# Optimization experiments

Measured on AMD Instinct MI355X. Metric: run time of the kernel, lower is better.

Reference implementation:

```python
import jax, jax.numpy as jnp
import numpy as np

B, N, OUT = 128, 4096, 64
PHI = (64, 128, 256)
RHO = (256, 128)
FMIN = jnp.finfo(jnp.float32).min


def _linear_params(key, fan_in, fan_out):
    # torch nn.Linear default init: U(-1/sqrt(fan_in), 1/sqrt(fan_in))
    kw, kb = jax.random.split(key)
    bound = 1.0 / np.sqrt(fan_in)
    w = jax.random.uniform(kw, (fan_in, fan_out), jnp.float32, -bound, bound)
    b = jax.random.uniform(kb, (fan_out,), jnp.float32, -bound, bound)
    return w, b


def setup_inputs() -> dict:
    key = jax.random.key(0)
    ks = jax.random.split(key, 8)
    points = jax.random.normal(ks[0], (B, N, 2), jnp.float32)
    lengths = jax.random.randint(ks[1], (B,), 1, N + 1, jnp.int32)
    w1, b1 = _linear_params(ks[2], 2, PHI[0])
    w2, b2 = _linear_params(ks[3], PHI[0], PHI[1])
    w3, b3 = _linear_params(ks[4], PHI[1], PHI[2])
    r1w, r1b = _linear_params(ks[5], PHI[2], RHO[0])
    r2w, r2b = _linear_params(ks[6], RHO[0], RHO[1])
    r3w, r3b = _linear_params(ks[7], RHO[1], OUT)
    return {"points": points, "lengths": lengths,
            "w1": w1, "b1": b1, "w2": w2, "b2": b2, "w3": w3, "b3": b3,
            "r1w": r1w, "r1b": r1b, "r2w": r2w, "r2b": r2b, "r3w": r3w, "r3b": r3b}


def reference(points, lengths, w1, b1, w2, b2, w3, b3, r1w, r1b, r2w, r2b, r3w, r3b):
    # mask[b, n] = n < lengths[b]   (pad_sequence equivalent)
    mask = jnp.arange(N)[None, :] < lengths[:, None]            # [B, N]
    # phi MLP: per-point 2 -> 64 -> 128 -> 256 with ReLU
    h = jax.nn.relu(jnp.einsum('bnd,df->bnf', points, w1) + b1)
    h = jax.nn.relu(jnp.einsum('bnd,df->bnf', h, w2) + b2)
    h = jax.nn.relu(jnp.einsum('bnd,df->bnf', h, w3) + b3)       # [B, N, 256]
    # masked max-pool over points (padding -> dtype min, matching masked_fill)
    h = jnp.where(mask[:, :, None], h, FMIN)
    agg = jnp.max(h, axis=1)                                     # [B, 256]
    # rho MLP: 256 -> 256 -> 128 -> OUT (ReLU on hidden layers only)
    z = jax.nn.relu(agg @ r1w + r1b)
    z = jax.nn.relu(z @ r2w + r2b)
    return z @ r3w + r3b                                         # [B, OUT]
```

## Files before the change

### kernel.cpp

```cpp
#include <hip/hip_runtime.h>
#include <hip/hip_fp16.h>

#define BB   128
#define NN   4096
#define OUTD 64
#define P1   64
#define P2   128
#define P3   256
#define R1   256
#define R2   128
#define CHUNK 64

typedef _Float16 half8 __attribute__((ext_vector_type(8)));
typedef _Float16 half4 __attribute__((ext_vector_type(4)));
typedef float    f32x4 __attribute__((ext_vector_type(4)));

#define AGG_OFF 0
#define W2F_OFF (BB * P3 * 4)
#define W3F_OFF (W2F_OFF + P2 * P1 * 2)

__global__ void prep_kernel(const float* __restrict__ w2, const float* __restrict__ w3,
                            unsigned char* ws) {
  int idx = blockIdx.x * 256 + threadIdx.x;
  if (idx < BB * P3) ((unsigned*)(ws + AGG_OFF))[idx] = 0u;
  _Float16* W2F = (_Float16*)(ws + W2F_OFF);
  _Float16* W3F = (_Float16*)(ws + W3F_OFF);
  if (idx < P1 * P2) {
    int f = idx >> 9, rem = idx & 511, l = rem >> 3, j = rem & 7;
    int mt = f >> 1, ks = f & 1;
    int ch = mt * 16 + (l & 15), k = ks * 32 + (l >> 4) * 8 + j;
    W2F[idx] = (_Float16)w2[k * P2 + ch];
  }
  int i2 = idx - P1 * P2;
  if (i2 >= 0 && i2 < P2 * P3) {
    int f = i2 >> 9, rem = i2 & 511, l = rem >> 3, j = rem & 7;
    int mt = f >> 2, ks = f & 3;
    int ch = mt * 16 + (l & 15), k = ks * 32 + (l >> 4) * 8 + j;
    W3F[i2] = (_Float16)w3[k * P3 + ch];
  }
}

__launch_bounds__(256, 3)
__global__ void phi_kernel(const float* __restrict__ pts, const int* __restrict__ lengths,
                           const float* __restrict__ w1, const float* __restrict__ b1,
                           const float* __restrict__ b2, const float* __restrict__ b3,
                           unsigned char* ws) {
  __shared__ __align__(16) _Float16 sH1[8][CHUNK][8];
  __shared__ __align__(16) _Float16 sH2[16][CHUNK][8];

  int b  = blockIdx.y;
  int c0 = blockIdx.x * CHUNK;
  int len = lengths[b];
  if (c0 >= len) return;
  int v = min(CHUNK, len - c0);

  int t = threadIdx.x;
  int w = t >> 6, l = t & 63;
  int ml = l & 15, q = l >> 4;

  const half8* W2F = (const half8*)(ws + W2F_OFF);
  const half8* W3F = (const half8*)(ws + W3F_OFF);

  half8 a2[2][2];
#pragma unroll
  for (int mt2 = 0; mt2 < 2; ++mt2)
#pragma unroll
    for (int ks = 0; ks < 2; ++ks)
      a2[mt2][ks] = W2F[((w * 2 + mt2) * 2 + ks) * 64 + l];
  half8 a3c[4];
#pragma unroll
  for (int ks = 0; ks < 4; ++ks)
    a3c[ks] = W3F[((w * 4 + 0) * 4 + ks) * 64 + l];

  {
    const float2* Pp = (const float2*)pts + (size_t)b * NN + c0;
    float2 xy = Pp[l];
    half8 h8[2];
#pragma unroll
    for (int j = 0; j < 16; ++j) {
      int jj = w * 16 + j;
      float h = fmaf(xy.y, w1[P1 + jj], fmaf(xy.x, w1[jj], b1[jj]));
      h8[j >> 3][j & 7] = (_Float16)fmaxf(h, 0.f);
    }
    *(half8*)&sH1[w * 2][l][0]     = h8[0];
    *(half8*)&sH1[w * 2 + 1][l][0] = h8[1];
  }
  __syncthreads();

  {
    f32x4 acc2[2][4] = {};
#pragma unroll
    for (int ks = 0; ks < 2; ++ks) {
      half8 bf[4];
#pragma unroll
      for (int nt = 0; nt < 4; ++nt)
        bf[nt] = *(const half8*)&sH1[ks * 4 + q][nt * 16 + ml][0];
#pragma unroll
      for (int mt2 = 0; mt2 < 2; ++mt2)
#pragma unroll
        for (int nt = 0; nt < 4; ++nt)
          acc2[mt2][nt] = __builtin_amdgcn_mfma_f32_16x16x32_f16(
              a2[mt2][ks], bf[nt], acc2[mt2][nt], 0, 0, 0);
    }
#pragma unroll
    for (int mt2 = 0; mt2 < 2; ++mt2) {
      float4 b2v = *(const float4*)&b2[(w * 2 + mt2) * 16 + q * 4];
#pragma unroll
      for (int nt = 0; nt < 4; ++nt) {
        half4 hp;
        hp[0] = (_Float16)fmaxf(acc2[mt2][nt][0] + b2v.x, 0.f);
        hp[1] = (_Float16)fmaxf(acc2[mt2][nt][1] + b2v.y, 0.f);
        hp[2] = (_Float16)fmaxf(acc2[mt2][nt][2] + b2v.z, 0.f);
        hp[3] = (_Float16)fmaxf(acc2[mt2][nt][3] + b2v.w, 0.f);
        *(half4*)&sH2[(w * 2 + mt2) * 2 + (q >> 1)][nt * 16 + ml][(q & 1) * 4] = hp;
      }
    }
  }
  __syncthreads();

  unsigned* aggU = (unsigned*)(ws + AGG_OFF) + b * P3;
  for (int s = 0; s < 4; ++s) {
    half8 a3n[4];
    if (s < 3) {
#pragma unroll
      for (int ks = 0; ks < 4; ++ks)
        a3n[ks] = W3F[((w * 4 + s + 1) * 4 + ks) * 64 + l];
    }
    float4 b3v = *(const float4*)&b3[(w * 4 + s) * 16 + q * 4];
    f32x4 acc3[4] = {};
#pragma unroll
    for (int ks = 0; ks < 4; ++ks)
#pragma unroll
      for (int nt = 0; nt < 4; ++nt) {
        half8 bf = *(const half8*)&sH2[ks * 4 + q][nt * 16 + ml][0];
        acc3[nt] = __builtin_amdgcn_mfma_f32_16x16x32_f16(
            a3c[ks], bf, acc3[nt], 0, 0, 0);
      }
    float rm[4] = {0.f, 0.f, 0.f, 0.f};
    float bb[4] = {b3v.x, b3v.y, b3v.z, b3v.w};
#pragma unroll
    for (int nt = 0; nt < 4; ++nt) {
      bool ok = (nt * 16 + ml) < v;
#pragma unroll
      for (int r = 0; r < 4; ++r) {
        float val = fmaxf(acc3[nt][r] + bb[r], 0.f);
        if (ok) rm[r] = fmaxf(rm[r], val);
      }
    }
#pragma unroll
    for (int r = 0; r < 4; ++r) {
      float m = rm[r];
      m = fmaxf(m, __shfl_xor(m, 1));
      m = fmaxf(m, __shfl_xor(m, 2));
      m = fmaxf(m, __shfl_xor(m, 4));
      m = fmaxf(m, __shfl_xor(m, 8));
      if (ml == 0)
        atomicMax(&aggU[(w * 4 + s) * 16 + q * 4 + r], __float_as_uint(m));
    }
#pragma unroll
    for (int ks = 0; ks < 4; ++ks) a3c[ks] = a3n[ks];
  }
}

__global__ void rho_kernel(const unsigned char* __restrict__ ws,
                           const float* __restrict__ r1w, const float* __restrict__ r1b,
                           const float* __restrict__ r2w, const float* __restrict__ r2b,
                           const float* __restrict__ r3w, const float* __restrict__ r3b,
                           float* __restrict__ out) {
  __shared__ float sa[R1], sz1[R1], sz2[R2];
  int b = blockIdx.x, t = threadIdx.x;
  const float* agg = (const float*)(ws + AGG_OFF) + b * P3;
  sa[t] = agg[t];
  __syncthreads();
  {
    float p0 = 0.f, p1 = 0.f, p2 = 0.f, p3 = 0.f;
#pragma unroll 8
    for (int k = 0; k < 64; ++k) {
      p0 = fmaf(sa[k],       r1w[k * R1 + t],         p0);
      p1 = fmaf(sa[k + 64],  r1w[(k + 64) * R1 + t],  p1);
      p2 = fmaf(sa[k + 128], r1w[(k + 128) * R1 + t], p2);
      p3 = fmaf(sa[k + 192], r1w[(k + 192) * R1 + t], p3);
    }
    sz1[t] = fmaxf(r1b[t] + ((p0 + p1) + (p2 + p3)), 0.f);
  }
  __syncthreads();
  if (t < R2) {
    float p0 = 0.f, p1 = 0.f, p2 = 0.f, p3 = 0.f;
#pragma unroll 8
    for (int k = 0; k < 64; ++k) {
      p0 = fmaf(sz1[k],       r2w[k * R2 + t],         p0);
      p1 = fmaf(sz1[k + 64],  r2w[(k + 64) * R2 + t],  p1);
      p2 = fmaf(sz1[k + 128], r2w[(k + 128) * R2 + t], p2);
      p3 = fmaf(sz1[k + 192], r2w[(k + 192) * R2 + t], p3);
    }
    sz2[t] = fmaxf(r2b[t] + ((p0 + p1) + (p2 + p3)), 0.f);
  }
  __syncthreads();
  if (t < OUTD) {
    float p0 = 0.f, p1 = 0.f;
#pragma unroll 8
    for (int k = 0; k < 64; ++k) {
      p0 = fmaf(sz2[k],      r3w[k * OUTD + t],        p0);
      p1 = fmaf(sz2[k + 64], r3w[(k + 64) * OUTD + t], p1);
    }
    out[b * OUTD + t] = r3b[t] + p0 + p1;
  }
}

extern "C" void kernel_launch(void* const* d_in, const int* in_sizes, int n_in,
                              void* d_out, int out_size, void* d_ws, size_t ws_size,
                              hipStream_t stream) {
  const float* pts     = (const float*)d_in[0];
  const int*   lengths = (const int*)d_in[1];
  const float* w1  = (const float*)d_in[2];
  const float* b1  = (const float*)d_in[3];
  const float* w2  = (const float*)d_in[4];
  const float* b2  = (const float*)d_in[5];
  const float* w3  = (const float*)d_in[6];
  const float* b3  = (const float*)d_in[7];
  const float* r1w = (const float*)d_in[8];
  const float* r1b = (const float*)d_in[9];
  const float* r2w = (const float*)d_in[10];
  const float* r2b = (const float*)d_in[11];
  const float* r3w = (const float*)d_in[12];
  const float* r3b = (const float*)d_in[13];
  unsigned char* ws = (unsigned char*)d_ws;

  prep_kernel<<<160, 256, 0, stream>>>(w2, w3, ws);
  phi_kernel<<<dim3(NN / CHUNK, BB), 256, 0, stream>>>(pts, lengths, w1, b1, b2, b3, ws);
  rho_kernel<<<BB, 256, 0, stream>>>(ws, r1w, r1b, r2w, r2b, r3w, r3b, (float*)d_out);
}
```

Measured before the change: 145.9 us.

## Fuse rho MLP into phi kernel via last-block-done counter per batch

Removes the separate rho kernel launch. Each phi block increments a per-batch atomic counter after its atomicMax updates, and the last block for that batch reads the aggregated vector and runs the three rho layers in reused shared memory. The layer-2 MFMA loop is also restructured to keep fewer accumulators live, and launch bounds are raised to 4 waves per SIMD for occupancy. The trade-offs are an added threadfence and atomic on every block, and a serialized rho tail running inside one block per batch.

```diff
diff --git a/kernel.cpp b/kernel.cpp
--- a/kernel.cpp
+++ b/kernel.cpp
@@ -18,11 +18,13 @@
 #define AGG_OFF 0
 #define W2F_OFF (BB * P3 * 4)
 #define W3F_OFF (W2F_OFF + P2 * P1 * 2)
+#define CNT_OFF (W3F_OFF + P2 * P3 * 2)
 
 __global__ void prep_kernel(const float* __restrict__ w2, const float* __restrict__ w3,
                             unsigned char* ws) {
   int idx = blockIdx.x * 256 + threadIdx.x;
   if (idx < BB * P3) ((unsigned*)(ws + AGG_OFF))[idx] = 0u;
+  if (idx < BB) ((int*)(ws + CNT_OFF))[idx] = 0;
   _Float16* W2F = (_Float16*)(ws + W2F_OFF);
   _Float16* W3F = (_Float16*)(ws + W3F_OFF);
   if (idx < P1 * P2) {
@@ -40,13 +42,17 @@
   }
 }
 
-__launch_bounds__(256, 3)
+__launch_bounds__(256, 4)
 __global__ void phi_kernel(const float* __restrict__ pts, const int* __restrict__ lengths,
                            const float* __restrict__ w1, const float* __restrict__ b1,
                            const float* __restrict__ b2, const float* __restrict__ b3,
-                           unsigned char* ws) {
+                           const float* __restrict__ r1w, const float* __restrict__ r1b,
+                           const float* __restrict__ r2w, const float* __restrict__ r2b,
+                           const float* __restrict__ r3w, const float* __restrict__ r3b,
+                           unsigned char* ws, float* __restrict__ out) {
   __shared__ __align__(16) _Float16 sH1[8][CHUNK][8];
   __shared__ __align__(16) _Float16 sH2[16][CHUNK][8];
+  __shared__ int sClose;
 
   int b  = blockIdx.y;
   int c0 = blockIdx.x * CHUNK;
@@ -87,33 +93,27 @@
   }
   __syncthreads();
 
-  {
-    f32x4 acc2[2][4] = {};
+#pragma unroll
+  for (int mt2 = 0; mt2 < 2; ++mt2) {
+    f32x4 acc2[4] = {};
 #pragma unroll
     for (int ks = 0; ks < 2; ++ks) {
-      half8 bf[4];
-#pragma unroll
-      for (int nt = 0; nt < 4; ++nt)
-        bf[nt] = *(const half8*)&sH1[ks * 4 + q][nt * 16 + ml][0];
-#pragma unroll
-      for (int mt2 = 0; mt2 < 2; ++mt2)
-#pragma unroll
-        for (int nt = 0; nt < 4; ++nt)
-          acc2[mt2][nt] = __builtin_amdgcn_mfma_f32_16x16x32_f16(
-              a2[mt2][ks], bf[nt], acc2[mt2][nt], 0, 0, 0);
-    }
-#pragma unroll
-    for (int mt2 = 0; mt2 < 2; ++mt2) {
-      float4 b2v = *(const float4*)&b2[(w * 2 + mt2) * 16 + q * 4];
 #pragma unroll
       for (int nt = 0; nt < 4; ++nt) {
-        half4 hp;
-        hp[0] = (_Float16)fmaxf(acc2[mt2][nt][0] + b2v.x, 0.f);
-        hp[1] = (_Float16)fmaxf(acc2[mt2][nt][1] + b2v.y, 0.f);
-        hp[2] = (_Float16)fmaxf(acc2[mt2][nt][2] + b2v.z, 0.f);
-        hp[3] = (_Float16)fmaxf(acc2[mt2][nt][3] + b2v.w, 0.f);
-        *(half4*)&sH2[(w * 2 + mt2) * 2 + (q >> 1)][nt * 16 + ml][(q & 1) * 4] = hp;
+        half8 bf = *(const half8*)&sH1[ks * 4 + q][nt * 16 + ml][0];
+        acc2[nt] = __builtin_amdgcn_mfma_f32_16x16x32_f16(
+            a2[mt2][ks], bf, acc2[nt], 0, 0, 0);
       }
+    }
+    float4 b2v = *(const float4*)&b2[(w * 2 + mt2) * 16 + q * 4];
+#pragma unroll
+    for (int nt = 0; nt < 4; ++nt) {
+      half4 hp;
+      hp[0] = (_Float16)fmaxf(acc2[nt][0] + b2v.x, 0.f);
+      hp[1] = (_Float16)fmaxf(acc2[nt][1] + b2v.y, 0.f);
+      hp[2] = (_Float16)fmaxf(acc2[nt][2] + b2v.z, 0.f);
+      hp[3] = (_Float16)fmaxf(acc2[nt][3] + b2v.w, 0.f);
+      *(half4*)&sH2[(w * 2 + mt2) * 2 + (q >> 1)][nt * 16 + ml][(q & 1) * 4] = hp;
     }
   }
   __syncthreads();
@@ -160,17 +160,22 @@
 #pragma unroll
     for (int ks = 0; ks < 4; ++ks) a3c[ks] = a3n[ks];
   }
-}
-
-__global__ void rho_kernel(const unsigned char* __restrict__ ws,
-                           const float* __restrict__ r1w, const float* __restrict__ r1b,
-                           const float* __restrict__ r2w, const float* __restrict__ r2b,
-                           const float* __restrict__ r3w, const float* __restrict__ r3b,
-                           float* __restrict__ out) {
-  __shared__ float sa[R1], sz1[R1], sz2[R2];
-  int b = blockIdx.x, t = threadIdx.x;
-  const float* agg = (const float*)(ws + AGG_OFF) + b * P3;
-  sa[t] = agg[t];
+
+  __threadfence();
+  __syncthreads();
+  if (t == 0) {
+    int nblk = (len + CHUNK - 1) >> 6;
+    int old = atomicAdd((int*)(ws + CNT_OFF) + b, 1);
+    sClose = (old == nblk - 1) ? 1 : 0;
+  }
+  __syncthreads();
+  if (!sClose) return;
+
+  float* sF  = (float*)sH1;
+  float* sa  = sF;
+  float* sz1 = sF + 256;
+  float* sz2 = sF + 512;
+  sa[t] = __uint_as_float(atomicMax(&aggU[t], 0u));
   __syncthreads();
   {
     float p0 = 0.f, p1 = 0.f, p2 = 0.f, p3 = 0.f;
@@ -227,6 +232,6 @@
   unsigned char* ws = (unsigned char*)d_ws;
 
   prep_kernel<<<160, 256, 0, stream>>>(w2, w3, ws);
-  phi_kernel<<<dim3(NN / CHUNK, BB), 256, 0, stream>>>(pts, lengths, w1, b1, b2, b3, ws);
-  rho_kernel<<<BB, 256, 0, stream>>>(ws, r1w, r1b, r2w, r2b, r3w, r3b, (float*)d_out);
+  phi_kernel<<<dim3(NN / CHUNK, BB), 256, 0, stream>>>(
+      pts, lengths, w1, b1, b2, b3, r1w, r1b, r2w, r2b, r3w, r3b, ws, (float*)d_out);
 }
```

Measured after the change: 421.1 us. 189% more time.
